# Performance work log

Measured on AMD Instinct MI355X. Metric: run time of the kernel, lower is better.

## Reference

```python
import jax, jax.numpy as jnp
import numpy as np
from jax import lax

DN = ('NCHW', 'OIHW', 'NCHW')

def conv2d(x, w, b=None, padding='SAME'):
    y = lax.conv_general_dilated(x, w, (1, 1), padding, dimension_numbers=DN)
    if b is not None:
        y = y + b[None, :, None, None]
    return y

def setup_inputs() -> dict:
    key = jax.random.key(0)
    ks = jax.random.split(key, 9)
    B, C, H, W = 8, 256, 64, 64
    s = lambda fan: 1.0 / np.sqrt(fan)
    return {
        'x': jax.random.normal(ks[0], (B, C, H, W), jnp.float32),
        'qkv_w': jax.random.normal(ks[1], (3 * C, C, 1, 1), jnp.float32) * s(C),
        'qkv_b': jnp.zeros((3 * C,), jnp.float32),
        'out_w': jax.random.normal(ks[2], (C, C, 1, 1), jnp.float32) * s(C),
        'out_b': jnp.zeros((C,), jnp.float32),
        'd1_w': jax.random.normal(ks[3], (8, 1, 3, 3), jnp.float32) * s(9),
        'd1_b': jnp.zeros((8,), jnp.float32),
        'd2_w': jax.random.normal(ks[4], (1, 8, 3, 3), jnp.float32) * s(72),
        'd2_b': jnp.zeros((1,), jnp.float32),
    }

def reference(x, qkv_w, qkv_b, out_w, out_b, d1_w, d1_b, d2_w, d2_b):
    B, C, H, W = x.shape
    N = H * W
    # gradient-energy (Laplacian) density proxy
    gray = x.mean(axis=1, keepdims=True)                      # [B,1,H,W]
    lap_k = jnp.array([[0., -1., 0.], [-1., 4., -1.], [0., -1., 0.]],
                      dtype=x.dtype).reshape(1, 1, 3, 3)
    lap = conv2d(gray, lap_k)                                 # [B,1,H,W]
    h = jax.nn.relu(conv2d(jnp.abs(lap), d1_w, d1_b))         # [B,8,H,W]
    density = jax.nn.sigmoid(conv2d(h, d2_w, d2_b))           # [B,1,H,W]
    # qkv via 1x1 conv == channel matmul
    qkv = jnp.einsum('oc,bchw->bohw', qkv_w[:, :, 0, 0], x) + qkv_b[None, :, None, None]
    q, k, v = jnp.split(qkv, 3, axis=1)                       # each [B,C,H,W]
    q = q.reshape(B, C, N).transpose(0, 2, 1)                 # [B,N,C]
    k = k.reshape(B, C, N)                                    # [B,C,N]
    v = v.reshape(B, C, N).transpose(0, 2, 1)                 # [B,N,C]
    attn = jnp.einsum('bnc,bcm->bnm', q, k) * (float(C) ** -0.5)  # [B,Nq,Nk]
    temperature = 1.0 + 2.0 * (1.0 - density.reshape(B, 1, N))    # per-key [B,1,Nk]
    attn = jax.nn.softmax(attn / temperature, axis=-1)
    out = jnp.einsum('bnm,bmc->bnc', attn, v)                 # [B,N,C]
    out = out.transpose(0, 2, 1).reshape(B, C, H, W)
    out = jnp.einsum('oc,bchw->bohw', out_w[:, :, 0, 0], out) + out_b[None, :, None, None]
    return out + x
```

## Files before the change

### kernel.cpp

```cpp
#include <hip/hip_runtime.h>
#include <hip/hip_bf16.h>

typedef __attribute__((ext_vector_type(8))) short s16x8;
typedef __attribute__((ext_vector_type(4))) float f32x4;
typedef __attribute__((ext_vector_type(16))) float f32x16;
typedef __attribute__((ext_vector_type(4))) unsigned short us4;
typedef __attribute__((ext_vector_type(4))) unsigned int u32x4;

#define MFMA16(a,b,c) __builtin_amdgcn_mfma_f32_16x16x32_bf16((a),(b),(c),0,0,0)
#define MFMA32(a,b,c) __builtin_amdgcn_mfma_f32_32x32x16_bf16((a),(b),(c),0,0,0)

__device__ __forceinline__ float b2f(unsigned short u){
  union{unsigned u; float f;} v; v.u = ((unsigned)u)<<16; return v.f;
}
__device__ __forceinline__ unsigned short f2b(float f){
  union{float f; unsigned u;} v; v.f = f;
  unsigned r = v.u + 0x7fffu + ((v.u>>16)&1u);
  return (unsigned short)(r>>16);
}

__device__ __forceinline__ void gl_lds16(const void* gp, void* lp){
  __builtin_amdgcn_global_load_lds((const __attribute__((address_space(1))) void*)gp,
                                   (__attribute__((address_space(3))) void*)lp, 16, 0, 0);
}

__device__ __forceinline__ void stage_64x256(void* lds, const unsigned short* g, int stride){
  const int t = threadIdx.x, wv = t>>6;
  #pragma unroll
  for (int i=0;i<8;++i){
    int ch = i*256 + t;
    int row = ch>>5, cc = ch&31, sc = cc ^ (row&7);
    gl_lds16((const char*)(g + (size_t)row*stride) + sc*16,
             (char*)lds + (((size_t)i*256 + wv*64)<<4));
  }
}
__device__ __forceinline__ void stage16KB(void* lds, const unsigned short* g){
  const int tid = threadIdx.x;
  #pragma unroll
  for (int i=0;i<2;++i){
    int ch = i*512 + tid;
    gl_lds16((const char*)(g + (size_t)ch*8), (char*)lds + (size_t)ch*16);
  }
}

__global__ void k_cvt(const float* __restrict__ src, unsigned short* __restrict__ dst){
  int i = blockIdx.x*256 + threadIdx.x;
  f32x4 v = *(const f32x4*)(src + (size_t)i*4);
  us4 o;
  #pragma unroll
  for (int r=0;r<4;++r) o[r] = f2b(v[r]);
  *(us4*)(dst + (size_t)i*4) = o;
}

__global__ void k_gray(const float* __restrict__ xg, float* __restrict__ gray){
  int b = blockIdx.y, n = blockIdx.x*256 + threadIdx.x;
  const float* p = xg + (size_t)b*256*4096 + n;
  float s0=0,s1=0,s2=0,s3=0;
  for (int c=0;c<256;c+=4){
    s0 += p[(size_t)c*4096];
    s1 += p[(size_t)(c+1)*4096];
    s2 += p[(size_t)(c+2)*4096];
    s3 += p[(size_t)(c+3)*4096];
  }
  gray[b*4096+n] = (s0+s1+s2+s3)*(1.f/256.f);
}

__global__ void k_lapabs(const float* __restrict__ gray, float* __restrict__ labs){
  int b = blockIdx.y, n = blockIdx.x*256 + threadIdx.x;
  int hh = n>>6, ww = n&63;
  const float* g = gray + b*4096;
  float c = g[n];
  float up = hh>0  ? g[n-64] : 0.f;
  float dn = hh<63 ? g[n+64] : 0.f;
  float lf = ww>0  ? g[n-1]  : 0.f;
  float rt = ww<63 ? g[n+1]  : 0.f;
  labs[b*4096+n] = fabsf(4.f*c - up - dn - lf - rt);
}

__global__ void k_h8(const float* __restrict__ labs, const float* __restrict__ w1,
                     const float* __restrict__ b1, float* __restrict__ hbuf){
  int b = blockIdx.y, n = blockIdx.x*256 + threadIdx.x;
  int hh = n>>6, ww = n&63;
  const float* L = labs + b*4096;
  float tap[9];
  #pragma unroll
  for (int dy=-1;dy<=1;++dy)
    #pragma unroll
    for (int dx=-1;dx<=1;++dx){
      int y=hh+dy, x2=ww+dx;
      tap[(dy+1)*3+dx+1] = (y>=0&&y<64&&x2>=0&&x2<64)? L[y*64+x2] : 0.f;
    }
  #pragma unroll
  for (int j=0;j<8;++j){
    float a = b1[j];
    #pragma unroll
    for (int k=0;k<9;++k) a += w1[j*9+k]*tap[k];
    hbuf[((size_t)(b*8+j))*4096 + n] = fmaxf(a, 0.f);
  }
}

__global__ void k_scale(const float* __restrict__ hbuf, const float* __restrict__ w2,
                        const float* __restrict__ b2_, float* __restrict__ sc){
  int b = blockIdx.y, n = blockIdx.x*256 + threadIdx.x;
  int hh = n>>6, ww = n&63;
  float a = b2_[0];
  #pragma unroll
  for (int j=0;j<8;++j){
    const float* H = hbuf + ((size_t)(b*8+j))*4096;
    #pragma unroll
    for (int dy=-1;dy<=1;++dy)
      #pragma unroll
      for (int dx=-1;dx<=1;++dx){
        int y=hh+dy, x2=ww+dx;
        if (y>=0&&y<64&&x2>=0&&x2<64) a += w2[j*9+(dy+1)*3+(dx+1)]*H[y*64+x2];
      }
  }
  float sig = 1.f/(1.f+__expf(-a));
  sc[b*4096+n] = 0.0625f/(3.f - 2.f*sig);
}

__global__ void k_transpose(const float* __restrict__ xg, unsigned short* __restrict__ Xtg){
  __shared__ unsigned short T[64*68];
  const int nb = blockIdx.x, cb = blockIdx.y, b = blockIdx.z;
  const int n0 = nb*64, c0 = cb*64;
  const int t = threadIdx.x;
  #pragma unroll
  for (int i=0;i<4;++i){
    int idx = i*256 + t;
    int c = idx>>4, k4 = idx&15;
    f32x4 v = *(const f32x4*)(xg + ((size_t)(b*256 + c0 + c))*4096 + n0 + k4*4);
    us4 o;
    #pragma unroll
    for (int r=0;r<4;++r) o[r] = f2b(v[r]);
    *(us4*)&T[c*68 + k4*4] = o;
  }
  __syncthreads();
  #pragma unroll
  for (int i=0;i<2;++i){
    int idx = i*256 + t;
    int n = idx>>3, ck = idx&7;
    unsigned short vv[8];
    #pragma unroll
    for (int j=0;j<8;++j) vv[j] = T[(ck*8+j)*68 + n];
    *(u32x4*)(Xtg + ((size_t)(b*4096 + n0 + n))*256 + c0 + ck*8) = *(const u32x4*)vv;
  }
}

__global__ __launch_bounds__(256,2) void k_gemm_qkv(const unsigned short* __restrict__ Wg,
    const unsigned short* __restrict__ Xtg, const float* __restrict__ biasg,
    unsigned short* __restrict__ Qo, unsigned short* __restrict__ Ko, unsigned short* __restrict__ Vto){
  __shared__ unsigned short Wl[64*256], Xl[64*256];
  const int nt_ = blockIdx.x, at = blockIdx.y, b = blockIdx.z;
  const int a0 = at*64, n0 = nt_*64;
  stage_64x256(Wl, Wg + (size_t)a0*256, 256);
  stage_64x256(Xl, Xtg + ((size_t)(b*4096 + n0))*256, 256);
  __syncthreads();
  const int t = threadIdx.x, w = t>>6, lane = t&63, lam = lane&15, lg = lane>>4;
  f32x4 zz = {0.f,0.f,0.f,0.f};
  f32x4 acc[4] = {zz,zz,zz,zz};
  #pragma unroll
  for (int u=0;u<8;++u){
    int ar = 16*w + lam;
    s16x8 af = *(const s16x8*)((const char*)Wl + ar*512 + ((64*u+16*lg) ^ ((ar&7)<<4)));
    #pragma unroll
    for (int ct=0;ct<4;++ct){
      int br = 16*ct + lam;
      s16x8 bf = *(const s16x8*)((const char*)Xl + br*512 + ((64*u+16*lg) ^ ((br&7)<<4)));
      acc[ct] = MFMA16(af, bf, acc[ct]);
    }
  }
  const int ob = a0 + 16*w + 4*lg;
  f32x4 bias4 = *(const f32x4*)(biasg + ob);
  #pragma unroll
  for (int ct=0;ct<4;++ct){
    int n = n0 + 16*ct + lam;
    us4 ov;
    #pragma unroll
    for (int r=0;r<4;++r) ov[r] = f2b(acc[ct][r] + bias4[r]);
    if (a0 < 256){
      *(us4*)(Qo + ((size_t)(b*4096 + n))*256 + ob) = ov;
    } else if (a0 < 512){
      int c4 = ob - 256;
      size_t idx = (((size_t)(b*128 + (n>>5))*1024) + (c4>>3)*32 + (n&31))*8 + (c4&7);
      *(us4*)(Ko + idx) = ov;
    } else {
      int c0v = ob - 512;
      size_t base = ((size_t)(b*128 + (n>>5))*1024 + ((n&31)>>3)*256)*8 + (n&7);
      #pragma unroll
      for (int r=0;r<4;++r)
        Vto[base + (size_t)(c0v+r)*8] = ov[r];
    }
  }
}

__global__ __launch_bounds__(512,2) void k_attn(const unsigned short* __restrict__ Qg,
    const unsigned short* __restrict__ Kg, const unsigned short* __restrict__ Vtg,
    const float* __restrict__ Sg, unsigned short* __restrict__ AOt){
  __shared__ __align__(16) char SL[132096];
  unsigned short* Kl = (unsigned short*)SL;
  unsigned short* Vl = (unsigned short*)(SL + 65536);
  float* mlb = (float*)(SL + 131072);
  float* Ob  = (float*)SL;

  const int tid = threadIdx.x, w = tid>>6, lane = tid&63, l31 = lane&31, h = lane>>5;
  const int g = w>>2;
  const int bid = blockIdx.x;
  const int b = bid&7, qt = bid>>3;
  const int qbase = qt*128 + (w&3)*32;

  const unsigned short* KgB = Kg  + (size_t)b*128*8192;
  const unsigned short* VtB = Vtg + (size_t)b*128*8192;
  const float* SgB = Sg + (size_t)b*4096 + g*2048;

  s16x8 qf[16];
  {
    const unsigned short* qp = Qg + ((size_t)(b*4096 + qbase + l31))*256 + 8*h;
    #pragma unroll
    for (int u=0;u<16;++u) qf[u] = *(const s16x8*)(qp + 16*u);
  }
  f32x16 oa[8];
  #pragma unroll
  for (int nb=0;nb<8;++nb)
    #pragma unroll
    for (int i=0;i<16;++i) oa[nb][i]=0.f;
  float m_run = -1.0e30f, l_run = 0.f;

  #define KBUF(bu,gr) (Kl + ((bu)*2+(gr))*8192)
  #define VBUF(bu,gr) (Vl + ((bu)*2+(gr))*8192)

  stage16KB(KBUF(0,0), KgB);
  stage16KB(KBUF(0,1), KgB + (size_t)64*8192);
  stage16KB(VBUF(0,0), VtB);
  stage16KB(VBUF(0,1), VtB + (size_t)64*8192);
  __syncthreads();

  int cur = 0;
  for (int t=0; t<64; ++t){
    if (t < 63){
      stage16KB(KBUF(cur^1,0), KgB + (size_t)(t+1)*8192);
      stage16KB(KBUF(cur^1,1), KgB + (size_t)(64+t+1)*8192);
      stage16KB(VBUF(cur^1,0), VtB + (size_t)(t+1)*8192);
      stage16KB(VBUF(cur^1,1), VtB + (size_t)(64+t+1)*8192);
    }
    const char* Kc = (const char*)KBUF(cur,g);
    const char* Vc = (const char*)VBUF(cur,g);

    f32x4 sv[4];
    {
      const float* Sp = SgB + t*32;
      #pragma unroll
      for (int j=0;j<4;++j) sv[j] = *(const f32x4*)(Sp + 8*j + 4*h);
    }

    f32x16 st;
    #pragma unroll
    for (int i=0;i<16;++i) st[i]=0.f;
    __builtin_amdgcn_s_setprio(1);
    #pragma unroll
    for (int u=0;u<16;++u){
      s16x8 kf = *(const s16x8*)(Kc + (((2*u+h)*32 + l31)<<4));
      st = MFMA32(kf, qf[u], st);
    }
    __builtin_amdgcn_s_setprio(0);

    float pm[16];
    #pragma unroll
    for (int j=0;j<4;++j)
      #pragma unroll
      for (int i=0;i<4;++i) pm[4*j+i] = st[4*j+i]*sv[j][i];

    float mx[8];
    #pragma unroll
    for (int i=0;i<8;++i) mx[i] = fmaxf(pm[i], pm[8+i]);
    #pragma unroll
    for (int i=0;i<4;++i) mx[i] = fmaxf(mx[i], mx[4+i]);
    float tmax = fmaxf(fmaxf(mx[0],mx[1]), fmaxf(mx[2],mx[3]));
    tmax = fmaxf(tmax, __shfl_xor(tmax, 32));

    if (__any(tmax > m_run + 8.0f)){
      float mnew = fmaxf(m_run, tmax);
      float fs = __expf(m_run - mnew);
      m_run = mnew;
      l_run *= fs;
      float fr[16];
      #pragma unroll
      for (int r=0;r<16;++r) fr[r] = __shfl(fs, (r&3)+8*(r>>2)+4*h);
      #pragma unroll
      for (int nb=0;nb<8;++nb)
        #pragma unroll
        for (int r=0;r<16;++r) oa[nb][r] *= fr[r];
    }
    #pragma unroll
    for (int i=0;i<16;++i) pm[i] = __expf(pm[i] - m_run);
    {
      float sm[8];
      #pragma unroll
      for (int i=0;i<8;++i) sm[i] = pm[i] + pm[8+i];
      #pragma unroll
      for (int i=0;i<4;++i) sm[i] += sm[4+i];
      float rs = (sm[0]+sm[1])+(sm[2]+sm[3]);
      rs += __shfl_xor(rs, 32);
      l_run += rs;
    }

    unsigned pq[8];
    #pragma unroll
    for (int j=0;j<4;++j){
      pq[2*j]   = (unsigned)f2b(pm[4*j])   | ((unsigned)f2b(pm[4*j+1])<<16);
      pq[2*j+1] = (unsigned)f2b(pm[4*j+2]) | ((unsigned)f2b(pm[4*j+3])<<16);
    }

    __builtin_amdgcn_s_setprio(1);
    #pragma unroll
    for (int ks=0;ks<2;++ks){
      const int j0 = 2*ks, j1 = 2*ks+1;
      unsigned s0 = h ? pq[2*j0]   : pq[2*j1];
      unsigned s1 = h ? pq[2*j0+1] : pq[2*j1+1];
      unsigned r0 = (unsigned)__shfl_xor((int)s0, 32);
      unsigned r1 = (unsigned)__shfl_xor((int)s1, 32);
      union { unsigned u[4]; s16x8 v; } pa;
      pa.u[0] = h ? r0 : pq[2*j0];
      pa.u[1] = h ? r1 : pq[2*j0+1];
      pa.u[2] = h ? pq[2*j1]   : r0;
      pa.u[3] = h ? pq[2*j1+1] : r1;
      #pragma unroll
      for (int nb=0;nb<8;++nb){
        s16x8 vf = *(const s16x8*)(Vc + (((2*ks+h)*256 + 32*nb + l31)<<4));
        oa[nb] = MFMA32(pa.v, vf, oa[nb]);
      }
    }
    __builtin_amdgcn_s_setprio(0);

    __syncthreads();
    cur ^= 1;
  }

  if (g == 1){
    if (h == 0){
      mlb[((w-4)*32 + l31)*2]   = m_run;
      mlb[((w-4)*32 + l31)*2+1] = l_run;
    }
    float* Ow = Ob + (size_t)(w-4)*32*256;
    #pragma unroll
    for (int nb=0;nb<8;++nb)
      #pragma unroll
      for (int r=0;r<16;++r){
        int qr = (r&3)+8*(r>>2)+4*h;
        Ow[qr*256 + 32*nb + l31] = oa[nb][r];
      }
  }
  __syncthreads();
  if (g == 0){
    const float* Or = Ob + (size_t)w*32*256;
    #pragma unroll
    for (int r=0;r<16;++r){
      int qr = (r&3)+8*(r>>2)+4*h;
      float m0r = __shfl(m_run, qr);
      float l0r = __shfl(l_run, qr);
      float m1r = mlb[(w*32+qr)*2];
      float l1r = mlb[(w*32+qr)*2+1];
      float M = fmaxf(m0r, m1r);
      float a0 = __expf(m0r - M), a1 = __expf(m1r - M);
      float inv = 1.f/(l0r*a0 + l1r*a1);
      a0 *= inv; a1 *= inv;
      unsigned short* dst = AOt + ((size_t)(b*4096 + qbase + qr))*256 + l31;
      #pragma unroll
      for (int nb=0;nb<8;++nb){
        float v = oa[nb][r]*a0 + Or[qr*256 + 32*nb + l31]*a1;
        dst[32*nb] = f2b(v);
      }
    }
  }
  #undef KBUF
  #undef VBUF
}

__global__ __launch_bounds__(256,2) void k_gemm_out(const unsigned short* __restrict__ Ag,
    const unsigned short* __restrict__ Bg, const float* __restrict__ biasg,
    const float* __restrict__ xg, float* __restrict__ outg){
  __shared__ unsigned short Al[64*256], Bl[64*256];
  const int at = blockIdx.x, bt = blockIdx.y, b = blockIdx.z;
  const int a0 = at*64, o0 = bt*64;
  stage_64x256(Al, Ag + ((size_t)(b*4096 + a0))*256, 256);
  stage_64x256(Bl, Bg + (size_t)o0*256, 256);
  __syncthreads();
  const int t = threadIdx.x, w = t>>6, lane = t&63, lam = lane&15, lg = lane>>4;
  f32x4 zz = {0.f,0.f,0.f,0.f};
  f32x4 acc[4] = {zz,zz,zz,zz};
  #pragma unroll
  for (int u=0;u<8;++u){
    int ar = 16*w + lam;
    s16x8 af = *(const s16x8*)((const char*)Al + ar*512 + ((64*u+16*lg) ^ ((ar&7)<<4)));
    #pragma unroll
    for (int ct=0;ct<4;++ct){
      int br = 16*ct + lam;
      s16x8 bf = *(const s16x8*)((const char*)Bl + br*512 + ((64*u+16*lg) ^ ((br&7)<<4)));
      acc[ct] = MFMA16(af, bf, acc[ct]);
    }
  }
  #pragma unroll
  for (int ct=0;ct<4;++ct){
    int o = o0 + 16*ct + lam;
    float ob_ = biasg[o];
    size_t base = ((size_t)(b*256 + o))*4096 + a0 + 16*w + 4*lg;
    f32x4 xv = *(const f32x4*)(xg + base);
    f32x4 ov;
    #pragma unroll
    for (int r=0;r<4;++r) ov[r] = acc[ct][r] + ob_ + xv[r];
    *(f32x4*)(outg + base) = ov;
  }
}

extern "C" void kernel_launch(void* const* d_in, const int* in_sizes, int n_in,
                              void* d_out, int out_size, void* d_ws, size_t ws_size,
                              hipStream_t stream){
  const float* x     = (const float*)d_in[0];
  const float* qkv_w = (const float*)d_in[1];
  const float* qkv_b = (const float*)d_in[2];
  const float* out_w = (const float*)d_in[3];
  const float* out_b = (const float*)d_in[4];
  const float* d1_w  = (const float*)d_in[5];
  const float* d1_b  = (const float*)d_in[6];
  const float* d2_w  = (const float*)d_in[7];
  const float* d2_b  = (const float*)d_in[8];
  float* out = (float*)d_out;

  char* p = (char*)d_ws;
  const size_t BIG = (size_t)8*4096*256*2;
  unsigned short* Xt = (unsigned short*)p; p += BIG;
  unsigned short* Q  = (unsigned short*)p; p += BIG;
  unsigned short* K  = (unsigned short*)p; p += BIG;
  unsigned short* Vt = (unsigned short*)p; p += BIG;
  unsigned short* Wq = (unsigned short*)p; p += (size_t)768*256*2;
  unsigned short* Wo = (unsigned short*)p; p += (size_t)256*256*2;
  float* gray = (float*)p; p += (size_t)8*4096*4;
  float* labs = (float*)p; p += (size_t)8*4096*4;
  float* hbuf = (float*)p; p += (size_t)8*8*4096*4;
  float* sc   = (float*)p; p += (size_t)8*4096*4;

  k_cvt      <<<dim3(192),    256, 0, stream>>>(qkv_w, Wq);
  k_cvt      <<<dim3(64),     256, 0, stream>>>(out_w, Wo);
  k_transpose<<<dim3(64,4,8), 256, 0, stream>>>(x, Xt);
  k_gray     <<<dim3(16,8),   256, 0, stream>>>(x, gray);
  k_lapabs   <<<dim3(16,8),   256, 0, stream>>>(gray, labs);
  k_h8       <<<dim3(16,8),   256, 0, stream>>>(labs, d1_w, d1_b, hbuf);
  k_scale    <<<dim3(16,8),   256, 0, stream>>>(hbuf, d2_w, d2_b, sc);
  k_gemm_qkv <<<dim3(64,12,8),256, 0, stream>>>(Wq, Xt, qkv_b, Q, K, Vt);
  k_attn     <<<dim3(256),    512, 0, stream>>>(Q, K, Vt, sc, Xt);
  k_gemm_out <<<dim3(64,4,8), 256, 0, stream>>>(Xt, Wo, out_b, x, out);
}
```

Baseline: 280.0 us.

## Fuse density pipeline into transpose and single kernel; switch attention softmax to exp2

The channel-mean reduction is folded into the transpose kernel, which already holds the bf16 tile and writes per-block partial sums. The four small density kernels are replaced by one per-batch kernel that keeps all intermediates in LDS, cutting launches and global round trips. The attention softmax now works in base 2: the scale constant absorbs log2(e), exponentials use exp2f, the rescale threshold is adjusted, exponentials are computed before the max check, and the bf16 pack uses v_cvt_pk_bf16_f32. In exchange, gray is now summed from bf16-rounded values, the hidden activations are stored as bf16, and the density kernel runs on only 8 blocks with serial stages.

Measured after the change: 287.7 us. 1.03x slower.

```diff
diff --git a/kernel.cpp b/kernel.cpp
--- a/kernel.cpp
+++ b/kernel.cpp
@@ -18,6 +18,11 @@
   unsigned r = v.u + 0x7fffu + ((v.u>>16)&1u);
   return (unsigned short)(r>>16);
 }
+__device__ __forceinline__ unsigned cvt_pk_bf16(float lo, float hi){
+  unsigned r;
+  asm volatile("v_cvt_pk_bf16_f32 %0, %1, %2" : "=v"(r) : "v"(lo), "v"(hi));
+  return r;
+}
 
 __device__ __forceinline__ void gl_lds16(const void* gp, void* lp){
   __builtin_amdgcn_global_load_lds((const __attribute__((address_space(1))) void*)gp,
@@ -52,75 +57,10 @@
   *(us4*)(dst + (size_t)i*4) = o;
 }
 
-__global__ void k_gray(const float* __restrict__ xg, float* __restrict__ gray){
-  int b = blockIdx.y, n = blockIdx.x*256 + threadIdx.x;
-  const float* p = xg + (size_t)b*256*4096 + n;
-  float s0=0,s1=0,s2=0,s3=0;
-  for (int c=0;c<256;c+=4){
-    s0 += p[(size_t)c*4096];
-    s1 += p[(size_t)(c+1)*4096];
-    s2 += p[(size_t)(c+2)*4096];
-    s3 += p[(size_t)(c+3)*4096];
-  }
-  gray[b*4096+n] = (s0+s1+s2+s3)*(1.f/256.f);
-}
-
-__global__ void k_lapabs(const float* __restrict__ gray, float* __restrict__ labs){
-  int b = blockIdx.y, n = blockIdx.x*256 + threadIdx.x;
-  int hh = n>>6, ww = n&63;
-  const float* g = gray + b*4096;
-  float c = g[n];
-  float up = hh>0  ? g[n-64] : 0.f;
-  float dn = hh<63 ? g[n+64] : 0.f;
-  float lf = ww>0  ? g[n-1]  : 0.f;
-  float rt = ww<63 ? g[n+1]  : 0.f;
-  labs[b*4096+n] = fabsf(4.f*c - up - dn - lf - rt);
-}
-
-__global__ void k_h8(const float* __restrict__ labs, const float* __restrict__ w1,
-                     const float* __restrict__ b1, float* __restrict__ hbuf){
-  int b = blockIdx.y, n = blockIdx.x*256 + threadIdx.x;
-  int hh = n>>6, ww = n&63;
-  const float* L = labs + b*4096;
-  float tap[9];
-  #pragma unroll
-  for (int dy=-1;dy<=1;++dy)
-    #pragma unroll
-    for (int dx=-1;dx<=1;++dx){
-      int y=hh+dy, x2=ww+dx;
-      tap[(dy+1)*3+dx+1] = (y>=0&&y<64&&x2>=0&&x2<64)? L[y*64+x2] : 0.f;
-    }
-  #pragma unroll
-  for (int j=0;j<8;++j){
-    float a = b1[j];
-    #pragma unroll
-    for (int k=0;k<9;++k) a += w1[j*9+k]*tap[k];
-    hbuf[((size_t)(b*8+j))*4096 + n] = fmaxf(a, 0.f);
-  }
-}
-
-__global__ void k_scale(const float* __restrict__ hbuf, const float* __restrict__ w2,
-                        const float* __restrict__ b2_, float* __restrict__ sc){
-  int b = blockIdx.y, n = blockIdx.x*256 + threadIdx.x;
-  int hh = n>>6, ww = n&63;
-  float a = b2_[0];
-  #pragma unroll
-  for (int j=0;j<8;++j){
-    const float* H = hbuf + ((size_t)(b*8+j))*4096;
-    #pragma unroll
-    for (int dy=-1;dy<=1;++dy)
-      #pragma unroll
-      for (int dx=-1;dx<=1;++dx){
-        int y=hh+dy, x2=ww+dx;
-        if (y>=0&&y<64&&x2>=0&&x2<64) a += w2[j*9+(dy+1)*3+(dx+1)]*H[y*64+x2];
-      }
-  }
-  float sig = 1.f/(1.f+__expf(-a));
-  sc[b*4096+n] = 0.0625f/(3.f - 2.f*sig);
-}
-
-__global__ void k_transpose(const float* __restrict__ xg, unsigned short* __restrict__ Xtg){
+__global__ void k_transpose(const float* __restrict__ xg, unsigned short* __restrict__ Xtg,
+                            float* __restrict__ gray4){
   __shared__ unsigned short T[64*68];
+  __shared__ float psum[4*64];
   const int nb = blockIdx.x, cb = blockIdx.y, b = blockIdx.z;
   const int n0 = nb*64, c0 = cb*64;
   const int t = threadIdx.x;
@@ -143,6 +83,95 @@
     #pragma unroll
     for (int j=0;j<8;++j) vv[j] = T[(ck*8+j)*68 + n];
     *(u32x4*)(Xtg + ((size_t)(b*4096 + n0 + n))*256 + c0 + ck*8) = *(const u32x4*)vv;
+  }
+  {
+    int j = t&63, q = t>>6;
+    float s = 0.f;
+    #pragma unroll
+    for (int c16=0;c16<16;++c16) s += b2f(T[(q*16+c16)*68 + j]);
+    psum[q*64 + j] = s;
+  }
+  __syncthreads();
+  if (t < 64){
+    float s = psum[t] + psum[64+t] + psum[128+t] + psum[192+t];
+    gray4[((size_t)(cb*8 + b))*4096 + n0 + t] = s;
+  }
+}
+
+__global__ __launch_bounds__(256) void k_density(const float* __restrict__ gray4,
+    const float* __restrict__ w1, const float* __restrict__ b1,
+    const float* __restrict__ w2, const float* __restrict__ b2_,
+    float* __restrict__ sc2){
+  __shared__ float gf[4096];
+  __shared__ float la[4096];
+  __shared__ unsigned short hb[8*4096];
+  const int b = blockIdx.x, t = threadIdx.x;
+  #pragma unroll
+  for (int i=0;i<16;++i){
+    int px = i*256 + t;
+    float s = gray4[(size_t)(0*8+b)*4096 + px] + gray4[(size_t)(1*8+b)*4096 + px]
+            + gray4[(size_t)(2*8+b)*4096 + px] + gray4[(size_t)(3*8+b)*4096 + px];
+    gf[px] = s * (1.f/256.f);
+  }
+  __syncthreads();
+  #pragma unroll
+  for (int i=0;i<16;++i){
+    int px = i*256 + t;
+    int hh = px>>6, ww = px&63;
+    float c = gf[px];
+    float up = hh>0  ? gf[px-64] : 0.f;
+    float dn = hh<63 ? gf[px+64] : 0.f;
+    float lf = ww>0  ? gf[px-1]  : 0.f;
+    float rt = ww<63 ? gf[px+1]  : 0.f;
+    la[px] = fabsf(4.f*c - up - dn - lf - rt);
+  }
+  __syncthreads();
+  float w1r[72], b1r[8];
+  #pragma unroll
+  for (int k=0;k<72;++k) w1r[k] = w1[k];
+  #pragma unroll
+  for (int j=0;j<8;++j) b1r[j] = b1[j];
+  #pragma unroll
+  for (int i=0;i<16;++i){
+    int px = i*256 + t;
+    int hh = px>>6, ww = px&63;
+    float tap[9];
+    #pragma unroll
+    for (int dy=-1;dy<=1;++dy)
+      #pragma unroll
+      for (int dx=-1;dx<=1;++dx){
+        int y=hh+dy, x2=ww+dx;
+        tap[(dy+1)*3+dx+1] = (y>=0&&y<64&&x2>=0&&x2<64)? la[y*64+x2] : 0.f;
+      }
+    #pragma unroll
+    for (int j=0;j<8;++j){
+      float a = b1r[j];
+      #pragma unroll
+      for (int k=0;k<9;++k) a += w1r[j*9+k]*tap[k];
+      hb[j*4096 + px] = f2b(fmaxf(a, 0.f));
+    }
+  }
+  __syncthreads();
+  float w2r[72], b20 = b2_[0];
+  #pragma unroll
+  for (int k=0;k<72;++k) w2r[k] = w2[k];
+  #pragma unroll
+  for (int i=0;i<16;++i){
+    int px = i*256 + t;
+    int hh = px>>6, ww = px&63;
+    float a = b20;
+    #pragma unroll
+    for (int j=0;j<8;++j){
+      #pragma unroll
+      for (int dy=-1;dy<=1;++dy)
+        #pragma unroll
+        for (int dx=-1;dx<=1;++dx){
+          int y=hh+dy, x2=ww+dx;
+          if (y>=0&&y<64&&x2>=0&&x2<64) a += w2r[j*9+(dy+1)*3+(dx+1)]*b2f(hb[j*4096 + y*64+x2]);
+        }
+    }
+    float sig = 1.f/(1.f+__expf(-a));
+    sc2[(size_t)b*4096 + px] = 0.09016844f/(3.f - 2.f*sig);
   }
 }
 
@@ -223,7 +252,7 @@
   for (int nb=0;nb<8;++nb)
     #pragma unroll
     for (int i=0;i<16;++i) oa[nb][i]=0.f;
-  float m_run = -1.0e30f, l_run = 0.f;
+  float m_run = 0.f, l_run = 0.f;
 
   #define KBUF(bu,gr) (Kl + ((bu)*2+(gr))*8192)
   #define VBUF(bu,gr) (Vl + ((bu)*2+(gr))*8192)
@@ -269,19 +298,24 @@
       #pragma unroll
       for (int i=0;i<4;++i) pm[4*j+i] = st[4*j+i]*sv[j][i];
 
+    float pe[16];
+    #pragma unroll
+    for (int i=0;i<16;++i) pe[i] = exp2f(pm[i] - m_run);
+
     float mx[8];
     #pragma unroll
     for (int i=0;i<8;++i) mx[i] = fmaxf(pm[i], pm[8+i]);
     #pragma unroll
     for (int i=0;i<4;++i) mx[i] = fmaxf(mx[i], mx[4+i]);
     float tmax = fmaxf(fmaxf(mx[0],mx[1]), fmaxf(mx[2],mx[3]));
-    tmax = fmaxf(tmax, __shfl_xor(tmax, 32));
-
-    if (__any(tmax > m_run + 8.0f)){
+    if (__any(tmax > m_run + 11.5415603f)){
+      tmax = fmaxf(tmax, __shfl_xor(tmax, 32));
       float mnew = fmaxf(m_run, tmax);
-      float fs = __expf(m_run - mnew);
+      float fs = exp2f(m_run - mnew);
       m_run = mnew;
       l_run *= fs;
+      #pragma unroll
+      for (int i=0;i<16;++i) pe[i] *= fs;
       float fr[16];
       #pragma unroll
       for (int r=0;r<16;++r) fr[r] = __shfl(fs, (r&3)+8*(r>>2)+4*h);
@@ -290,12 +324,10 @@
         #pragma unroll
         for (int r=0;r<16;++r) oa[nb][r] *= fr[r];
     }
-    #pragma unroll
-    for (int i=0;i<16;++i) pm[i] = __expf(pm[i] - m_run);
     {
       float sm[8];
       #pragma unroll
-      for (int i=0;i<8;++i) sm[i] = pm[i] + pm[8+i];
+      for (int i=0;i<8;++i) sm[i] = pe[i] + pe[8+i];
       #pragma unroll
       for (int i=0;i<4;++i) sm[i] += sm[4+i];
       float rs = (sm[0]+sm[1])+(sm[2]+sm[3]);
@@ -306,8 +338,8 @@
     unsigned pq[8];
     #pragma unroll
     for (int j=0;j<4;++j){
-      pq[2*j]   = (unsigned)f2b(pm[4*j])   | ((unsigned)f2b(pm[4*j+1])<<16);
-      pq[2*j+1] = (unsigned)f2b(pm[4*j+2]) | ((unsigned)f2b(pm[4*j+3])<<16);
+      pq[2*j]   = cvt_pk_bf16(pe[4*j],   pe[4*j+1]);
+      pq[2*j+1] = cvt_pk_bf16(pe[4*j+2], pe[4*j+3]);
     }
 
     __builtin_amdgcn_s_setprio(1);
@@ -360,7 +392,7 @@
       float m1r = mlb[(w*32+qr)*2];
       float l1r = mlb[(w*32+qr)*2+1];
       float M = fmaxf(m0r, m1r);
-      float a0 = __expf(m0r - M), a1 = __expf(m1r - M);
+      float a0 = exp2f(m0r - M), a1 = exp2f(m1r - M);
       float inv = 1.f/(l0r*a0 + l1r*a1);
       a0 *= inv; a1 *= inv;
       unsigned short* dst = AOt + ((size_t)(b*4096 + qbase + qr))*256 + l31;
@@ -433,18 +465,13 @@
   unsigned short* Vt = (unsigned short*)p; p += BIG;
   unsigned short* Wq = (unsigned short*)p; p += (size_t)768*256*2;
   unsigned short* Wo = (unsigned short*)p; p += (size_t)256*256*2;
-  float* gray = (float*)p; p += (size_t)8*4096*4;
-  float* labs = (float*)p; p += (size_t)8*4096*4;
-  float* hbuf = (float*)p; p += (size_t)8*8*4096*4;
-  float* sc   = (float*)p; p += (size_t)8*4096*4;
+  float* gray4 = (float*)p; p += (size_t)4*8*4096*4;
+  float* sc    = (float*)p; p += (size_t)8*4096*4;
 
   k_cvt      <<<dim3(192),    256, 0, stream>>>(qkv_w, Wq);
   k_cvt      <<<dim3(64),     256, 0, stream>>>(out_w, Wo);
-  k_transpose<<<dim3(64,4,8), 256, 0, stream>>>(x, Xt);
-  k_gray     <<<dim3(16,8),   256, 0, stream>>>(x, gray);
-  k_lapabs   <<<dim3(16,8),   256, 0, stream>>>(gray, labs);
-  k_h8       <<<dim3(16,8),   256, 0, stream>>>(labs, d1_w, d1_b, hbuf);
-  k_scale    <<<dim3(16,8),   256, 0, stream>>>(hbuf, d2_w, d2_b, sc);
+  k_transpose<<<dim3(64,4,8), 256, 0, stream>>>(x, Xt, gray4);
+  k_density  <<<dim3(8),      256, 0, stream>>>(gray4, d1_w, d1_b, d2_w, d2_b, sc);
   k_gemm_qkv <<<dim3(64,12,8),256, 0, stream>>>(Wq, Xt, qkv_b, Q, K, Vt);
   k_attn     <<<dim3(256),    512, 0, stream>>>(Q, K, Vt, sc, Xt);
   k_gemm_out <<<dim3(64,4,8), 256, 0, stream>>>(Xt, Wo, out_b, x, out);
```
